# Optimization experiments

Hardware: AMD Instinct MI355X
Metric: run time of the kernel (lower is better)

## Reference

```python
import jax, jax.numpy as jnp
import numpy as np

N_NODES = 200000
N_EDGES = 3200000
F_IN, HID, N_CLS = 128, 35, 10


def setup_inputs() -> dict:
    key = jax.random.key(0)
    k = jax.random.split(key, 5)
    x = jax.random.normal(k[0], (N_NODES, F_IN), dtype=jnp.float32)
    edge_index = jax.random.randint(k[1], (2, N_EDGES), 0, N_NODES, dtype=jnp.int64)
    W1 = jax.random.normal(k[2], (F_IN, HID), dtype=jnp.float32) / np.sqrt(F_IN)
    b1 = jnp.zeros((HID,), dtype=jnp.float32)
    W2 = jax.random.normal(k[3], (HID, N_CLS), dtype=jnp.float32) / np.sqrt(HID)
    b2 = jnp.zeros((N_CLS,), dtype=jnp.float32)
    return {"x": x, "edge_index": edge_index, "W1": W1, "b1": b1, "W2": W2, "b2": b2}


def _gcn_conv(x, W, b, row, col, norm, n_nodes):
    # GCNConv: linear transform, then normalized neighbor aggregation (scatter-add)
    h = x @ W                               # [N, d_out]
    msg = h[row] * norm[:, None]            # gather along edges, [E+N, d_out]
    agg = jax.ops.segment_sum(msg, col, num_segments=n_nodes)
    return agg + b


def reference(x, edge_index, W1, b1, W2, b2):
    n = x.shape[0]
    loop = jnp.arange(n, dtype=edge_index.dtype)
    row = jnp.concatenate([edge_index[0], loop])  # sources (+ self loops)
    col = jnp.concatenate([edge_index[1], loop])  # targets (+ self loops)
    deg = jax.ops.segment_sum(jnp.ones_like(col, dtype=x.dtype), col, num_segments=n)
    dinv = jnp.where(deg > 0, deg ** -0.5, 0.0)
    norm = dinv[row] * dinv[col]                  # D^{-1/2} A D^{-1/2} edge weights

    h = _gcn_conv(x, W1, b1, row, col, norm, n)
    h = jax.nn.relu(h)
    # F.dropout with training=self.training: identity at inference
    out = _gcn_conv(h, W2, b2, row, col, norm, n)
    return jax.nn.log_softmax(out, axis=1)
```

## Files before the change

kernel.cpp:

```cpp
#include <hip/hip_runtime.h>

#define NN    200000
#define F_IN  128
#define HID   35
#define LD1   36
#define LD2   12
#define NCLS  10
#define NPB   256
#define NB    782
#define CAP   5120
#define EPT   32

static __device__ inline unsigned short f2bf(float f) {
    unsigned u = __float_as_uint(f);
    u = (u + 0x7FFFu + ((u >> 16) & 1u)) >> 16;
    return (unsigned short)u;
}
static __device__ inline unsigned pk2(float a, float b) {
    return (unsigned)f2bf(a) | ((unsigned)f2bf(b) << 16);
}
static __device__ inline float bf2f(unsigned short h) {
    return __uint_as_float((unsigned)h << 16);
}


__global__ void k_initcur(int* __restrict__ gcur) {
    int t = threadIdx.x;
    if (t < NB) gcur[t] = t * CAP;
}

__global__ __launch_bounds__(256)
void k_bucket(const int* __restrict__ row, const int* __restrict__ col, int E,
              int* __restrict__ gcur, unsigned* __restrict__ bkt) {
    __shared__ int hist[NB];
    __shared__ int basev[NB];
    int t = threadIdx.x;
    long e0 = (long)blockIdx.x * (256 * EPT);
    for (int i = t; i < NB; i += 256) hist[i] = 0;
    __syncthreads();
    int cols[EPT];
#pragma unroll
    for (int i = 0; i < EPT; ++i) {
        long e = e0 + (long)i * 256 + t;
        if (e < E) {
            int c = col[e];
            cols[i] = c;
            atomicAdd(&hist[c >> 8], 1);
        } else cols[i] = -1;
    }
    __syncthreads();
    for (int i = t; i < NB; i += 256) {
        int h = hist[i];
        basev[i] = (h > 0) ? atomicAdd(&gcur[i], h) : 0;
        hist[i] = 0;
    }
    __syncthreads();
#pragma unroll
    for (int i = 0; i < EPT; ++i) {
        int c = cols[i];
        if (c >= 0) {
            long e = e0 + (long)i * 256 + t;
            int r = row[e];
            int b = c >> 8;
            int pos = basev[b] + atomicAdd(&hist[b], 1);
            if (pos < NB * CAP) bkt[pos] = (unsigned)r | ((unsigned)(c & 255) << 18);
        }
    }
}

__global__ __launch_bounds__(256)
void k_sort(unsigned* __restrict__ bkt, const int* __restrict__ gcur,
            int* __restrict__ obeg, int* __restrict__ oend,
            float* __restrict__ dinv, int n) {
    __shared__ unsigned est[CAP];
    __shared__ int hist[NPB];
    __shared__ int cur[NPB];
    __shared__ int sc[NPB];
    int b = blockIdx.x, t = threadIdx.x;
    int ec = gcur[b] - b * CAP;
    if (ec > CAP) ec = CAP;
    unsigned* ep = bkt + (size_t)b * CAP;
    hist[t] = 0;
    __syncthreads();
    for (int e = t; e < ec; e += 256) {
        unsigned p = ep[e];
        est[e] = p;
        atomicAdd(&hist[p >> 18], 1);
    }
    __syncthreads();
    sc[t] = hist[t];
    __syncthreads();
    for (int d = 1; d < NPB; d <<= 1) {
        int add = (t >= d) ? sc[t - d] : 0;
        __syncthreads();
        sc[t] += add;
        __syncthreads();
    }
    int excl = sc[t] - hist[t];
    cur[t] = excl;
    int i = b * NPB + t;
    if (i < n) {
        obeg[i] = b * CAP + excl;
        oend[i] = b * CAP + excl + hist[t];
        dinv[i] = rsqrtf((float)(hist[t] + 1));
    }
    __syncthreads();
    for (int e = t; e < ec; e += 256) {
        unsigned p = est[e];
        int lc = p >> 18;
        int pos = atomicAdd(&cur[lc], 1);
        ep[pos] = p & 0x3FFFF;
    }
}


__global__ void k_gemm1(const float* __restrict__ x, const float* __restrict__ W1,
                        const float* __restrict__ dinv,
                        unsigned short* __restrict__ hs1A,
                        unsigned short* __restrict__ hs1B, int n) {
    int i = blockIdx.x * blockDim.x + threadIdx.x;
    if (i >= n) return;
    float acc[HID];
#pragma unroll
    for (int j = 0; j < HID; ++j) acc[j] = 0.f;
    const float4* xr = (const float4*)(x + (size_t)i * F_IN);
    for (int k4 = 0; k4 < F_IN / 4; ++k4) {
        float4 xv = xr[k4];
        const float* w = W1 + (size_t)(k4 * 4) * HID;
#pragma unroll
        for (int j = 0; j < HID; ++j)
            acc[j] += xv.x * w[j] + xv.y * w[HID + j] + xv.z * w[2 * HID + j] + xv.w * w[3 * HID + j];
    }
    float d = dinv[i];
    unsigned* oa = (unsigned*)(hs1A + (size_t)i * 32);
#pragma unroll
    for (int j = 0; j < 16; ++j) oa[j] = pk2(acc[2 * j] * d, acc[2 * j + 1] * d);
    unsigned* ob = (unsigned*)(hs1B + (size_t)i * 4);
    ob[0] = pk2(acc[32] * d, acc[33] * d);
    ob[1] = pk2(acc[34] * d, 0.f);
}

__global__ void k_agg1(const int* __restrict__ obeg, const int* __restrict__ oend,
                       const unsigned* __restrict__ srow,
                       const unsigned short* __restrict__ A,
                       const unsigned short* __restrict__ Bf,
                       float* __restrict__ acc1, int n) {
    int wid = (blockIdx.x * blockDim.x + threadIdx.x) >> 6;
    int lane = threadIdx.x & 63;
    if (wid >= n) return;
    int half = lane >> 5;
    int fl = lane & 31;
    bool bact = fl < 4;
    int beg = obeg[wid], end = oend[wid];
    float acc  = (half == 0) ? bf2f(A[(size_t)wid * 32 + fl]) : 0.f;
    float accb = (half == 0 && bact) ? bf2f(Bf[(size_t)wid * 4 + fl]) : 0.f;
    int j = beg + half;
    for (; j + 6 < end; j += 8) {
        int r0 = srow[j], r1 = srow[j + 2], r2 = srow[j + 4], r3 = srow[j + 6];
        float a0 = bf2f(A[(size_t)r0 * 32 + fl]);
        float a1 = bf2f(A[(size_t)r1 * 32 + fl]);
        float a2 = bf2f(A[(size_t)r2 * 32 + fl]);
        float a3 = bf2f(A[(size_t)r3 * 32 + fl]);
        acc += (a0 + a1) + (a2 + a3);
        if (bact) {
            float b0 = bf2f(Bf[(size_t)r0 * 4 + fl]);
            float b1 = bf2f(Bf[(size_t)r1 * 4 + fl]);
            float b2v = bf2f(Bf[(size_t)r2 * 4 + fl]);
            float b3 = bf2f(Bf[(size_t)r3 * 4 + fl]);
            accb += (b0 + b1) + (b2v + b3);
        }
    }
    for (; j < end; j += 2) {
        int r = srow[j];
        acc += bf2f(A[(size_t)r * 32 + fl]);
        if (bact) accb += bf2f(Bf[(size_t)r * 4 + fl]);
    }
    acc  += __shfl_xor(acc, 32);
    accb += __shfl_xor(accb, 32);
    if (lane < 32) acc1[(size_t)wid * LD1 + lane] = acc;
    if (lane < 4)  acc1[(size_t)wid * LD1 + 32 + lane] = accb;
}


__global__ void k_layer2(const float* __restrict__ acc1, const float* __restrict__ dinv,
                         const float* __restrict__ b1, const float* __restrict__ W2,
                         unsigned short* __restrict__ hs2b, int n) {
    int i = blockIdx.x * blockDim.x + threadIdx.x;
    if (i >= n) return;
    float d = dinv[i];
    const float4* a = (const float4*)(acc1 + (size_t)i * LD1);
    float4 tq[9];
#pragma unroll
    for (int q = 0; q < 9; ++q) tq[q] = a[q];
    const float* tf = (const float*)tq;
    float h[HID];
#pragma unroll
    for (int k = 0; k < HID; ++k) {
        float v = tf[k] * d + b1[k];
        h[k] = v > 0.f ? v : 0.f;
    }
    float o[NCLS];
#pragma unroll
    for (int j = 0; j < NCLS; ++j) o[j] = 0.f;
#pragma unroll
    for (int k = 0; k < HID; ++k) {
#pragma unroll
        for (int j = 0; j < NCLS; ++j) o[j] += h[k] * W2[k * NCLS + j];
    }
    unsigned* dst = (unsigned*)(hs2b + (size_t)i * LD2);
#pragma unroll
    for (int j = 0; j < 5; ++j) dst[j] = pk2(o[2 * j] * d, o[2 * j + 1] * d);
    dst[5] = 0u;
}

__global__ void k_agg2o(const int* __restrict__ obeg, const int* __restrict__ oend,
                        const unsigned* __restrict__ srow,
                        const unsigned short* __restrict__ hs2b,
                        const float* __restrict__ dinv, const float* __restrict__ b2,
                        float* __restrict__ out, int n) {
    int wid = (blockIdx.x * blockDim.x + threadIdx.x) >> 6;
    int lane = threadIdx.x & 63;
    if (wid >= n) return;
    int sub = lane >> 4;
    int f = lane & 15;
    bool act = f < LD2;
    int beg = obeg[wid], end = oend[wid];
    float acc = (lane < LD2) ? bf2f(hs2b[(size_t)wid * LD2 + lane]) : 0.f;
    for (int j = beg + sub; j < end; j += 4) {
        int r = srow[j];
        if (act) acc += bf2f(hs2b[(size_t)r * LD2 + f]);
    }
    acc += __shfl_down(acc, 32);
    acc += __shfl_down(acc, 16);
    float d = dinv[wid];
    float v = (lane < NCLS) ? acc * d + b2[lane] : -1e30f;
    float m = v;
    m = fmaxf(m, __shfl_xor(m, 1, 16));
    m = fmaxf(m, __shfl_xor(m, 2, 16));
    m = fmaxf(m, __shfl_xor(m, 4, 16));
    m = fmaxf(m, __shfl_xor(m, 8, 16));
    float e = (lane < NCLS) ? expf(v - m) : 0.f;
    float s = e;
    s += __shfl_xor(s, 1, 16);
    s += __shfl_xor(s, 2, 16);
    s += __shfl_xor(s, 4, 16);
    s += __shfl_xor(s, 8, 16);
    if (lane < NCLS) out[(size_t)wid * NCLS + lane] = v - m - logf(s);
}

extern "C" void kernel_launch(void* const* d_in, const int* in_sizes, int n_in,
                              void* d_out, int out_size, void* d_ws, size_t ws_size,
                              hipStream_t stream) {
    const float* x  = (const float*)d_in[0];
    const int*   ei = (const int*)d_in[1];
    const float* W1 = (const float*)d_in[2];
    const float* b1 = (const float*)d_in[3];
    const float* W2 = (const float*)d_in[4];
    const float* b2 = (const float*)d_in[5];
    float* out = (float*)d_out;

    const int n = in_sizes[0] / F_IN;
    const int E = in_sizes[1] / 2;
    const int* row = ei;
    const int* col = ei + E;

    unsigned*       bkt  = (unsigned*)d_ws;
    int*            gcur = (int*)d_ws + 4003840;
    int*            obeg = (int*)d_ws + 4004864;
    int*            oend = (int*)d_ws + 4204864;
    float*          dinv = (float*)d_ws + 4404864;
    unsigned short* hs1A = (unsigned short*)((unsigned*)d_ws + 4604864);
    unsigned short* hs1B = (unsigned short*)((unsigned*)d_ws + 7804864);
    float*          acc1 = (float*)d_ws + 8204864;
    unsigned short* hs2b = hs1A;

    const int B = 256;
    const int nbk = (E + B * EPT - 1) / (B * EPT);

    k_initcur<<<1, 1024, 0, stream>>>(gcur);
    k_bucket<<<nbk, B, 0, stream>>>(row, col, E, gcur, bkt);
    k_sort<<<NB, B, 0, stream>>>(bkt, gcur, obeg, oend, dinv, n);

    k_gemm1<<<(n + B - 1) / B, B, 0, stream>>>(x, W1, dinv, hs1A, hs1B, n);
    k_agg1<<<(n * 64 + B - 1) / B, B, 0, stream>>>(obeg, oend, bkt, hs1A, hs1B, acc1, n);
    k_layer2<<<(n + B - 1) / B, B, 0, stream>>>(acc1, dinv, b1, W2, hs2b, n);
    k_agg2o<<<(n * 64 + B - 1) / B, B, 0, stream>>>(obeg, oend, bkt, hs2b, dinv, b2, out, n);
}
```

Before: 372.2 us.

## Vectorize neighbor gathers in aggregation kernels with 16 edges per wave

Both aggregation kernels now assign one edge to each of 16 lane slots and a feature chunk to each of 4 lane groups. Each lane loads 16 bytes (layer 1) or 8 bytes (layer 2) with wide vector loads instead of one bf16 per lane, and the next edge index is prefetched one iteration ahead. Partial sums are reduced with xor shuffles at the end, and log_softmax is computed on packed 4-wide values. The aim is fewer load instructions and more edges in flight per wave. The cost is a longer shuffle reduction and idle lanes when a node has few neighbors.

```diff
diff --git a/kernel.cpp b/kernel.cpp
--- a/kernel.cpp
+++ b/kernel.cpp
@@ -19,9 +19,8 @@
 static __device__ inline unsigned pk2(float a, float b) {
     return (unsigned)f2bf(a) | ((unsigned)f2bf(b) << 16);
 }
-static __device__ inline float bf2f(unsigned short h) {
-    return __uint_as_float((unsigned)h << 16);
-}
+static __device__ inline float bflo(unsigned u) { return __uint_as_float(u << 16); }
+static __device__ inline float bfhi(unsigned u) { return __uint_as_float(u & 0xFFFF0000u); }
 
 
 __global__ void k_initcur(int* __restrict__ gcur) {
@@ -148,37 +147,54 @@
     int wid = (blockIdx.x * blockDim.x + threadIdx.x) >> 6;
     int lane = threadIdx.x & 63;
     if (wid >= n) return;
-    int half = lane >> 5;
-    int fl = lane & 31;
-    bool bact = fl < 4;
+    int s = lane & 15;
+    int g = lane >> 4;
     int beg = obeg[wid], end = oend[wid];
-    float acc  = (half == 0) ? bf2f(A[(size_t)wid * 32 + fl]) : 0.f;
-    float accb = (half == 0 && bact) ? bf2f(Bf[(size_t)wid * 4 + fl]) : 0.f;
-    int j = beg + half;
-    for (; j + 6 < end; j += 8) {
-        int r0 = srow[j], r1 = srow[j + 2], r2 = srow[j + 4], r3 = srow[j + 6];
-        float a0 = bf2f(A[(size_t)r0 * 32 + fl]);
-        float a1 = bf2f(A[(size_t)r1 * 32 + fl]);
-        float a2 = bf2f(A[(size_t)r2 * 32 + fl]);
-        float a3 = bf2f(A[(size_t)r3 * 32 + fl]);
-        acc += (a0 + a1) + (a2 + a3);
-        if (bact) {
-            float b0 = bf2f(Bf[(size_t)r0 * 4 + fl]);
-            float b1 = bf2f(Bf[(size_t)r1 * 4 + fl]);
-            float b2v = bf2f(Bf[(size_t)r2 * 4 + fl]);
-            float b3 = bf2f(Bf[(size_t)r3 * 4 + fl]);
-            accb += (b0 + b1) + (b2v + b3);
-        }
-    }
-    for (; j < end; j += 2) {
-        int r = srow[j];
-        acc += bf2f(A[(size_t)r * 32 + fl]);
-        if (bact) accb += bf2f(Bf[(size_t)r * 4 + fl]);
-    }
-    acc  += __shfl_xor(acc, 32);
-    accb += __shfl_xor(accb, 32);
-    if (lane < 32) acc1[(size_t)wid * LD1 + lane] = acc;
-    if (lane < 4)  acc1[(size_t)wid * LD1 + 32 + lane] = accb;
+    float a0=0.f,a1=0.f,a2=0.f,a3=0.f,a4=0.f,a5=0.f,a6=0.f,a7=0.f;
+    float b0=0.f,b1=0.f,b2=0.f;
+    int e = beg + s;
+    unsigned idx = (e < end) ? srow[e] : 0xFFFFFFFFu;
+    for (int base = beg; base < end; base += 16) {
+        int en = base + 16 + s;
+        unsigned nidx = (en < end) ? srow[en] : 0xFFFFFFFFu;
+        bool v = (idx != 0xFFFFFFFFu);
+        unsigned r = v ? idx : (unsigned)wid;
+        uint4 av = *(const uint4*)(A + ((size_t)r << 5) + (g << 3));
+        if (v) {
+            a0 += bflo(av.x); a1 += bfhi(av.x);
+            a2 += bflo(av.y); a3 += bfhi(av.y);
+            a4 += bflo(av.z); a5 += bfhi(av.z);
+            a6 += bflo(av.w); a7 += bfhi(av.w);
+        }
+        if (lane < 16 && v) {
+            uint2 bv = *(const uint2*)(Bf + ((size_t)r << 2));
+            b0 += bflo(bv.x); b1 += bfhi(bv.x); b2 += bflo(bv.y);
+        }
+        idx = nidx;
+    }
+#pragma unroll
+    for (int d = 1; d < 16; d <<= 1) {
+        a0 += __shfl_xor(a0, d); a1 += __shfl_xor(a1, d);
+        a2 += __shfl_xor(a2, d); a3 += __shfl_xor(a3, d);
+        a4 += __shfl_xor(a4, d); a5 += __shfl_xor(a5, d);
+        a6 += __shfl_xor(a6, d); a7 += __shfl_xor(a7, d);
+        b0 += __shfl_xor(b0, d); b1 += __shfl_xor(b1, d); b2 += __shfl_xor(b2, d);
+    }
+    if (s == 0) {
+        uint4 sv = *(const uint4*)(A + ((size_t)wid << 5) + (g << 3));
+        a0 += bflo(sv.x); a1 += bfhi(sv.x);
+        a2 += bflo(sv.y); a3 += bfhi(sv.y);
+        a4 += bflo(sv.z); a5 += bfhi(sv.z);
+        a6 += bflo(sv.w); a7 += bfhi(sv.w);
+        float* o = acc1 + (size_t)wid * LD1 + (g << 3);
+        *(float4*)o       = make_float4(a0, a1, a2, a3);
+        *(float4*)(o + 4) = make_float4(a4, a5, a6, a7);
+    }
+    if (lane == 0) {
+        uint2 sb = *(const uint2*)(Bf + ((size_t)wid << 2));
+        b0 += bflo(sb.x); b1 += bfhi(sb.x); b2 += bflo(sb.y);
+        *(float4*)(acc1 + (size_t)wid * LD1 + 32) = make_float4(b0, b1, b2, 0.f);
+    }
 }
 
 
@@ -215,37 +231,67 @@
 
 __global__ void k_agg2o(const int* __restrict__ obeg, const int* __restrict__ oend,
                         const unsigned* __restrict__ srow,
-                        const unsigned short* __restrict__ hs2b,
+                        const unsigned short* __restrict__ H,
                         const float* __restrict__ dinv, const float* __restrict__ b2,
                         float* __restrict__ out, int n) {
     int wid = (blockIdx.x * blockDim.x + threadIdx.x) >> 6;
     int lane = threadIdx.x & 63;
     if (wid >= n) return;
-    int sub = lane >> 4;
-    int f = lane & 15;
-    bool act = f < LD2;
+    int s = lane & 15;
+    int g = lane >> 4;
     int beg = obeg[wid], end = oend[wid];
-    float acc = (lane < LD2) ? bf2f(hs2b[(size_t)wid * LD2 + lane]) : 0.f;
-    for (int j = beg + sub; j < end; j += 4) {
-        int r = srow[j];
-        if (act) acc += bf2f(hs2b[(size_t)r * LD2 + f]);
-    }
-    acc += __shfl_down(acc, 32);
-    acc += __shfl_down(acc, 16);
-    float d = dinv[wid];
-    float v = (lane < NCLS) ? acc * d + b2[lane] : -1e30f;
-    float m = v;
-    m = fmaxf(m, __shfl_xor(m, 1, 16));
-    m = fmaxf(m, __shfl_xor(m, 2, 16));
-    m = fmaxf(m, __shfl_xor(m, 4, 16));
-    m = fmaxf(m, __shfl_xor(m, 8, 16));
-    float e = (lane < NCLS) ? expf(v - m) : 0.f;
-    float s = e;
-    s += __shfl_xor(s, 1, 16);
-    s += __shfl_xor(s, 2, 16);
-    s += __shfl_xor(s, 4, 16);
-    s += __shfl_xor(s, 8, 16);
-    if (lane < NCLS) out[(size_t)wid * NCLS + lane] = v - m - logf(s);
+    float a0=0.f,a1=0.f,a2=0.f,a3=0.f;
+    int e = beg + s;
+    unsigned idx = (e < end) ? srow[e] : 0xFFFFFFFFu;
+    for (int base = beg; base < end; base += 16) {
+        int en = base + 16 + s;
+        unsigned nidx = (en < end) ? srow[en] : 0xFFFFFFFFu;
+        bool v = (idx != 0xFFFFFFFFu);
+        unsigned r = v ? idx : (unsigned)wid;
+        uint2 hv = make_uint2(0u, 0u);
+        if (g < 3) hv = *(const uint2*)(H + (size_t)r * LD2 + (g << 2));
+        if (v) {
+            a0 += bflo(hv.x); a1 += bfhi(hv.x);
+            a2 += bflo(hv.y); a3 += bfhi(hv.y);
+        }
+        idx = nidx;
+    }
+#pragma unroll
+    for (int d = 1; d < 16; d <<= 1) {
+        a0 += __shfl_xor(a0, d); a1 += __shfl_xor(a1, d);
+        a2 += __shfl_xor(a2, d); a3 += __shfl_xor(a3, d);
+    }
+    float v0 = -1e30f, v1 = -1e30f, v2 = -1e30f, v3 = -1e30f;
+    float dn = dinv[wid];
+    if (s == 0 && g < 3) {
+        uint2 sv = *(const uint2*)(H + (size_t)wid * LD2 + (g << 2));
+        a0 += bflo(sv.x); a1 += bfhi(sv.x);
+        a2 += bflo(sv.y); a3 += bfhi(sv.y);
+        int f0 = g << 2;
+        v0 = a0 * dn + b2[f0];
+        v1 = a1 * dn + b2[f0 + 1];
+        if (f0 + 2 < NCLS) {
+            v2 = a2 * dn + b2[f0 + 2];
+            v3 = a3 * dn + b2[f0 + 3];
+        }
+    }
+    float m = fmaxf(fmaxf(v0, v1), fmaxf(v2, v3));
+    m = fmaxf(m, __shfl_xor(m, 16));
+    m = fmaxf(m, __shfl_xor(m, 32));
+    float e0 = (v0 > -1e29f) ? expf(v0 - m) : 0.f;
+    float e1 = (v1 > -1e29f) ? expf(v1 - m) : 0.f;
+    float e2 = (v2 > -1e29f) ? expf(v2 - m) : 0.f;
+    float e3 = (v3 > -1e29f) ? expf(v3 - m) : 0.f;
+    float sm = (e0 + e1) + (e2 + e3);
+    sm += __shfl_xor(sm, 16);
+    sm += __shfl_xor(sm, 32);
+    if (s == 0 && g < 3) {
+        float l = logf(sm);
+        int f0 = g << 2;
+        float* o = out + (size_t)wid * NCLS + f0;
+        *(float2*)o = make_float2(v0 - m - l, v1 - m - l);
+        if (f0 + 2 < NCLS) *(float2*)(o + 2) = make_float2(v2 - m - l, v3 - m - l);
+    }
 }
 
 extern "C" void kernel_launch(void* const* d_in, const int* in_sizes, int n_in,
```

After: 325.4 us. 1.14x faster.
